# Kernel optimization log

Hardware: AMD Instinct MI355X
Metric: run time of the kernel (lower is better)

## Reference

```python
import jax, jax.numpy as jnp
import numpy as np

B, N = 4, 20                        # batch, qubits
L = int(np.ceil(np.log2(N)))        # 5 layers, one 4x4 generator each


def setup_inputs():
    key = jax.random.key(0)
    k1, k2, k3, k4 = jax.random.split(key, 4)
    psi_re = jax.random.normal(k1, (B, 2 ** N), dtype=jnp.float32)
    psi_im = jax.random.normal(k2, (B, 2 ** N), dtype=jnp.float32)
    nrm = jnp.sqrt(jnp.sum(psi_re ** 2 + psi_im ** 2, axis=1, keepdims=True))
    psi_re, psi_im = psi_re / nrm, psi_im / nrm   # normalized quantum state
    H_re = jax.random.normal(k3, (L, 4, 4), dtype=jnp.float32)
    H_im = jax.random.normal(k4, (L, 4, 4), dtype=jnp.float32)
    return {"psi_re": psi_re, "psi_im": psi_im, "H_re": H_re, "H_im": H_im}


def _make_unitary(A):
    # torch.matrix_exp(A - A^H): expm of an anti-Hermitian generator via eigh
    G = A - A.conj().T
    w, V = jnp.linalg.eigh(-1j * G)            # G = i * Hermitian
    return (V * jnp.exp(1j * w)) @ V.conj().T  # expm(G), unitary


def _apply_gate(T, U4, axes):
    # contract 4x4 gate (reshaped [2,2,2,2]) onto two qubit axes of tensor T
    T = jnp.tensordot(U4, T, axes=((2, 3), axes))
    return jnp.moveaxis(T, (0, 1), axes)


def _gate_pairs(nq):
    pairs = [(2 * i, 2 * i + 1) for i in range(nq // 2)]
    if nq > 2:
        pairs += [(2 * i + 1, (2 * i + 2) % nq) for i in range(nq // 2)]
    return pairs


def _forward(psi_re, psi_im, H_re, H_im):
    psi = (psi_re + 1j * psi_im).astype(jnp.complex64).reshape((B,) + (2,) * N)
    H = (H_re + 1j * H_im).astype(jnp.complex64)
    state, is_dm, nq = psi, False, N
    for layer in range(L):
        U = _make_unitary(H[layer]).reshape(2, 2, 2, 2)
        Uc = U.conj()
        # _2local_conv: brick pattern of the same 2-qubit gate
        for (a, b) in _gate_pairs(nq):
            state = _apply_gate(state, U, (1 + a, 1 + b))
            if is_dm:  # density matrix: also apply U* on bra axes
                state = _apply_gate(state, Uc, (1 + nq + a, 1 + nq + b))
        # _2local_pool: measuring qubits 0..nq//2-1 with index shifting removes
        # the even-indexed qubits -> partial trace over them
        if nq >= 2:
            traced = [2 * i for i in range(nq // 2)]
            kept = [q for q in range(nq) if q not in traced]
            t, k = len(traced), len(kept)
            if is_dm:
                perm = (0,) + tuple(1 + q for q in kept) + tuple(1 + q for q in traced) \
                     + tuple(1 + nq + q for q in kept) + tuple(1 + nq + q for q in traced)
                r = jnp.transpose(state, perm).reshape(B, 2 ** k, 2 ** t, 2 ** k, 2 ** t)
                state = jnp.einsum('bitjt->bij', r).reshape((B,) + (2,) * k + (2,) * k)
            else:
                perm = (0,) + tuple(1 + q for q in traced) + tuple(1 + q for q in kept)
                p = jnp.transpose(state, perm).reshape(B, 2 ** t, 2 ** k)
                state = jnp.einsum('bti,btj->bij', p, p.conj()).reshape((B,) + (2,) * k + (2,) * k)
                is_dm = True
            nq = k
    # final state.measure(0): reduced 1-qubit density matrix, take P(outcome 0)
    r = state.reshape(B, 2, 2 ** (nq - 1), 2, 2 ** (nq - 1))
    rho0 = jnp.einsum('birjr->bij', r)
    return rho0[:, 0, 0].real


def reference(psi_re, psi_im, H_re, H_im):
    return _forward(psi_re, psi_im, H_re, H_im)
```

## Files before the change

kernel.cpp:

```cpp
#include <hip/hip_runtime.h>
#include <math.h>


__device__ __forceinline__ float2 cmul(float2 a, float2 b) {
  return make_float2(a.x * b.x - a.y * b.y, a.x * b.y + a.y * b.x);
}
__device__ __forceinline__ float2 cmadd(float2 acc, float2 a, float2 b) {
  acc.x = fmaf(a.x, b.x, fmaf(-a.y, b.y, acc.x));
  acc.y = fmaf(a.x, b.y, fmaf(a.y, b.x, acc.y));
  return acc;
}
__device__ __forceinline__ float2 cmaddc(float2 acc, float2 a, float2 b) {
  acc.x = fmaf(a.x, b.x, fmaf(a.y, b.y, acc.x));
  acc.y = fmaf(a.y, b.x, fmaf(-a.x, b.y, acc.y));
  return acc;
}
__device__ __forceinline__ int pad(int e) { return e + (e >> 4); }

__device__ __forceinline__ unsigned spread(unsigned v) {
  v = (v | (v << 8)) & 0x00FF00FFu;
  v = (v | (v << 4)) & 0x0F0F0F0Fu;
  v = (v | (v << 2)) & 0x33333333u;
  v = (v | (v << 1)) & 0x55555555u;
  return v;
}
__device__ __forceinline__ unsigned spread2(unsigned v) { return spread(spread(v)); }
__device__ __forceinline__ int ins(int x, int p) {
  return ((x >> p) << (p + 1)) | (x & ((1 << p) - 1));
}

__device__ __forceinline__ void gate4(float2& v0, float2& v1, float2& v2, float2& v3,
                                      const float2 (&U)[16]) {
  float2 n0 = cmul(U[0], v0);  n0 = cmadd(n0, U[1], v1);  n0 = cmadd(n0, U[2], v2);  n0 = cmadd(n0, U[3], v3);
  float2 n1 = cmul(U[4], v0);  n1 = cmadd(n1, U[5], v1);  n1 = cmadd(n1, U[6], v2);  n1 = cmadd(n1, U[7], v3);
  float2 n2 = cmul(U[8], v0);  n2 = cmadd(n2, U[9], v1);  n2 = cmadd(n2, U[10], v2); n2 = cmadd(n2, U[11], v3);
  float2 n3 = cmul(U[12], v0); n3 = cmadd(n3, U[13], v1); n3 = cmadd(n3, U[14], v2); n3 = cmadd(n3, U[15], v3);
  v0 = n0; v1 = n1; v2 = n2; v3 = n3;
}

template <int NG>
__device__ __forceinline__ void gate16n(float2 (&v)[16], const float2 (&U)[16]) {
#pragma unroll
  for (int g = 0; g < 4; g++)
    gate4(v[g * 4 + 0], v[g * 4 + 1], v[g * 4 + 2], v[g * 4 + 3], U);
#pragma unroll
  for (int lo = 0; lo < 4; lo++)
    gate4(v[lo], v[lo + 4], v[lo + 8], v[lo + 12], U);
  if (NG == 3) {
#pragma unroll
    for (int b3 = 0; b3 < 2; b3++)
#pragma unroll
      for (int b0 = 0; b0 < 2; b0++) {
        int j = b3 * 8 + b0;
        gate4(v[j], v[j + 2], v[j + 4], v[j + 6], U);
      }
  }
}

__device__ __forceinline__ void apply_gate_tile13(float2* t, const float2 (&U)[16],
                                                  int pa, int pb, int tid) {
  int p0 = pa < pb ? pa : pb;
  int p1 = pa < pb ? pb : pa;
  int m0 = (1 << p0) - 1, m1 = (1 << p1) - 1;
  int ia = 1 << pa, ib = 1 << pb;
#pragma unroll
  for (int g = tid; g < 2048; g += 512) {
    int idx = ((g & ~m0) << 1) | (g & m0);
    idx = ((idx & ~m1) << 1) | (idx & m1);
    int e0 = pad(idx), e1 = pad(idx | ib), e2 = pad(idx | ia), e3 = pad(idx | ia | ib);
    float2 v0 = t[e0], v1 = t[e1], v2 = t[e2], v3 = t[e3];
    gate4(v0, v1, v2, v3, U);
    t[e0] = v0; t[e1] = v1; t[e2] = v2; t[e3] = v3;
  }
}

template <int NG>
__device__ __forceinline__ void phase4_l0(float2* t, const float2 (&U)[16],
                                          int p0, int p1, int p2, int p3, int tid) {
  int o0 = 1 << p0, o1 = 1 << p1, o2 = 1 << p2, o3 = 1 << p3;
  int idx = ins(ins(ins(ins(tid, p0), p1), p2), p3);
  float2 v[16];
#pragma unroll
  for (int j = 0; j < 16; j++) {
    int off = ((j & 1) ? o0 : 0) + ((j & 2) ? o1 : 0) + ((j & 4) ? o2 : 0) + ((j & 8) ? o3 : 0);
    v[j] = t[pad(idx + off)];
  }
  gate16n<NG>(v, U);
#pragma unroll
  for (int j = 0; j < 16; j++) {
    int off = ((j & 1) ? o0 : 0) + ((j & 2) ? o1 : 0) + ((j & 4) ? o2 : 0) + ((j & 8) ? o3 : 0);
    t[pad(idx + off)] = v[j];
  }
}

template <int NG>
__device__ __forceinline__ void phase4_pool(float2* w, const float2 (&U)[16],
                                            int a_lo, int a_hi, int c_lo, int c_hi,
                                            int o0, int o1, int o2, int o3, int tid) {
  int uu = tid & 7, ss = (tid >> 3) & 7, t_lo = tid >> 6;
  int u = ins(ins(uu, a_lo), a_hi);
  int s = ins(ins(ss, c_lo), c_hi);
  int base = t_lo * 1056 + s * 33 + u;
  float2 v[16];
#pragma unroll
  for (int j = 0; j < 16; j++) {
    int off = ((j & 1) ? o0 : 0) + ((j & 2) ? o1 : 0) + ((j & 4) ? o2 : 0) + ((j & 8) ? o3 : 0);
    v[j] = w[base + off];
  }
  gate16n<NG>(v, U);
#pragma unroll
  for (int j = 0; j < 16; j++) {
    int off = ((j & 1) ? o0 : 0) + ((j & 2) ? o1 : 0) + ((j & 4) ? o2 : 0) + ((j & 8) ? o3 : 0);
    w[base + off] = v[j];
  }
}

__device__ __forceinline__ void pool_p3(float2* w, const float2 (&U)[16], int tid) {
#pragma unroll
  for (int it = 0; it < 2; it++) {
    int h = tid + it * 512;
    int uu = h & 7, ss = (h >> 3) & 15, t_lo = h >> 7;
    int base = t_lo * 1056 + (ss << 1) * 33 + (uu << 2);
    float2 v[8];
    v[0] = w[base];      v[1] = w[base + 1];
    v[4] = w[base + 2];  v[5] = w[base + 3];
    v[2] = w[base + 33]; v[3] = w[base + 34];
    v[6] = w[base + 35]; v[7] = w[base + 36];
    gate4(v[0], v[1], v[2], v[3], U);
    gate4(v[4], v[5], v[6], v[7], U);
    gate4(v[0], v[2], v[4], v[6], U);
    gate4(v[1], v[3], v[5], v[7], U);
    w[base] = v[0];      w[base + 1] = v[1];
    w[base + 2] = v[4];  w[base + 3] = v[5];
    w[base + 33] = v[2]; w[base + 34] = v[3];
    w[base + 35] = v[6]; w[base + 36] = v[7];
  }
}

__global__ __launch_bounds__(320) void expm_kernel(const float* __restrict__ Hre,
                                                   const float* __restrict__ Him,
                                                   float2* __restrict__ Uout) {
  int wave = threadIdx.x >> 6;
  int lane = threadIdx.x & 63;
  if (wave >= 5 || lane >= 16) return;
  int l = wave;
  int r = lane >> 2, c = lane & 3;
  double tr = (double)Hre[l * 16 + r * 4 + c] - (double)Hre[l * 16 + c * 4 + r];
  double ti = (double)Him[l * 16 + r * 4 + c] + (double)Him[l * 16 + c * 4 + r];
  double a = sqrt(tr * tr + ti * ti);
  a += __shfl_xor(a, 1, 64);
  a += __shfl_xor(a, 2, 64);
  double nrm = fmax(a, __shfl_xor(a, 4, 64));
  nrm = fmax(nrm, __shfl_xor(nrm, 8, 64));
  int s = 0;
  while (nrm > 0.25 && s < 60) { nrm *= 0.5; s++; }
  double sc = ldexp(1.0, -s);
  tr *= sc; ti *= sc;
  double id = (r == c) ? 1.0 : 0.0;
  double er = id, ei = 0.0, pr = id, pi = 0.0;
  for (int k = 1; k <= 16; k++) {
    double qr = 0.0, qi = 0.0;
#pragma unroll
    for (int m = 0; m < 4; m++) {
      double pmr = __shfl(pr, r * 4 + m, 64);
      double pmi = __shfl(pi, r * 4 + m, 64);
      double tmr = __shfl(tr, m * 4 + c, 64);
      double tmi = __shfl(ti, m * 4 + c, 64);
      qr = fma(pmr, tmr, fma(-pmi, tmi, qr));
      qi = fma(pmr, tmi, fma(pmi, tmr, qi));
    }
    double inv = 1.0 / (double)k;
    pr = qr * inv; pi = qi * inv;
    er += pr; ei += pi;
  }
  for (int it = 0; it < s; it++) {
    double qr = 0.0, qi = 0.0;
#pragma unroll
    for (int m = 0; m < 4; m++) {
      double amr = __shfl(er, r * 4 + m, 64);
      double ami = __shfl(ei, r * 4 + m, 64);
      double bmr = __shfl(er, m * 4 + c, 64);
      double bmi = __shfl(ei, m * 4 + c, 64);
      qr = fma(amr, bmr, fma(-ami, bmi, qr));
      qi = fma(amr, bmi, fma(ami, bmr, qi));
    }
    er = qr; ei = qi;
  }
  Uout[l * 16 + lane] = make_float2((float)er, (float)ei);
}

__global__ __launch_bounds__(512, 4) void l0_pass1(const float* __restrict__ pre,
                                                   const float* __restrict__ pim,
                                                   const float2* __restrict__ Umat,
                                                   float2* __restrict__ state) {
  extern __shared__ float2 tile[];
  int tid = threadIdx.x;
  int bid = blockIdx.x;
  int b = bid >> 7, hi = bid & 127;
  size_t base = ((size_t)b << 20) | ((size_t)hi << 13);
  float2 U[16];
#pragma unroll
  for (int k = 0; k < 16; k++) U[k] = Umat[k];
  for (int e = tid; e < 8192; e += 512)
    tile[pad(e)] = make_float2(pre[base + e], pim[base + e]);
  __syncthreads();
  phase4_l0<3>(tile, U, 0, 1, 2, 3, tid);   __syncthreads();
  phase4_l0<3>(tile, U, 4, 5, 6, 7, tid);   __syncthreads();
  phase4_l0<3>(tile, U, 8, 9, 10, 11, tid); __syncthreads();
  phase4_l0<2>(tile, U, 3, 4, 7, 8, tid);   __syncthreads();
  for (int e = tid; e < 8192; e += 512) state[base + e] = tile[pad(e)];
}

__global__ __launch_bounds__(512, 4) void l0_pass2(const float2* __restrict__ Umat,
                                                   float2* __restrict__ state) {
  extern __shared__ float2 tile[];
  int tid = threadIdx.x;
  int bid = blockIdx.x;
  int b = bid >> 7, mid = bid & 127;
  size_t base = ((size_t)b << 20) | ((size_t)mid << 4);
  float2 U[16];
#pragma unroll
  for (int k = 0; k < 16; k++) U[k] = Umat[k];
  for (int e = tid; e < 8192; e += 512) {
    size_t a = base + (((size_t)(e >> 4)) << 11) + (size_t)(e & 15);
    tile[pad(e)] = state[a];
  }
  __syncthreads();
  phase4_l0<3>(tile, U, 5, 6, 7, 8, tid);    __syncthreads();
  phase4_l0<3>(tile, U, 9, 10, 11, 12, tid); __syncthreads();
  phase4_l0<2>(tile, U, 4, 5, 8, 9, tid);    __syncthreads();
  apply_gate_tile13(tile, U, 0, 12, tid);    __syncthreads();
  for (int e = tid; e < 8192; e += 512) {
    size_t a = base + (((size_t)(e >> 4)) << 11) + (size_t)(e & 15);
    state[a] = tile[pad(e)];
  }
}

__global__ __launch_bounds__(512, 4) void pool_l1(const float2* __restrict__ Umat,
                                                  const float2* __restrict__ state,
                                                  float2* __restrict__ partial) {
  extern __shared__ float2 w[];
  int tid = threadIdx.x;
  int bid = blockIdx.x;
  int b = bid >> 7, thi = bid & 127;
  size_t bbase = (size_t)b << 20;
  float2 U[16];
#pragma unroll
  for (int k = 0; k < 16; k++) U[k] = Umat[16 + k];
  unsigned tbase = spread((unsigned)(thi << 3)) << 1;
  for (int e = tid; e < 8192; e += 512) {
    int u = e & 31, s = (e >> 5) & 31, t_lo = e >> 10;
    unsigned addr = tbase | (spread((unsigned)t_lo) << 1) | spread2((unsigned)u)
                  | (spread2((unsigned)s) << 2);
    w[t_lo * 1056 + s * 33 + u] = state[bbase + (size_t)addr];
  }
  __syncthreads();
  phase4_pool<3>(w, U, 3, 4, 3, 4, 8, 264, 16, 528, tid); __syncthreads();
  phase4_pool<3>(w, U, 1, 2, 1, 2, 2, 66, 4, 132, tid);   __syncthreads();
  pool_p3(w, U, tid);                                     __syncthreads();
  phase4_pool<2>(w, U, 0, 3, 2, 4, 132, 8, 528, 1, tid);  __syncthreads();
  int wv = tid >> 6, lane = tid & 63;
  int u0 = (lane >> 3) << 2, v0 = (lane & 7) << 2;
  float2 acc[4][4];
#pragma unroll
  for (int i = 0; i < 4; i++)
#pragma unroll
    for (int j = 0; j < 4; j++) acc[i][j] = make_float2(0.f, 0.f);
  {
    int tb = wv * 1056;
#pragma unroll 4
    for (int s = 0; s < 32; s++) {
      int row = tb + s * 33;
      float2 x[4], y[4];
#pragma unroll
      for (int i = 0; i < 4; i++) { x[i] = w[row + u0 + i]; y[i] = w[row + v0 + i]; }
#pragma unroll
      for (int i = 0; i < 4; i++)
#pragma unroll
        for (int j = 0; j < 4; j++) acc[i][j] = cmaddc(acc[i][j], x[i], y[j]);
    }
  }
  __syncthreads();
  if (wv > 0) {
#pragma unroll
    for (int i = 0; i < 4; i++)
#pragma unroll
      for (int j = 0; j < 4; j++)
        w[(wv - 1) * 1024 + (u0 + i) * 32 + (v0 + j)] = acc[i][j];
  }
  __syncthreads();
  if (wv == 0) {
    float2* outp = partial + ((size_t)bid << 10);
#pragma unroll
    for (int i = 0; i < 4; i++)
#pragma unroll
      for (int j = 0; j < 4; j++) {
        float2 a = acc[i][j];
#pragma unroll
        for (int k = 0; k < 7; k++) {
          float2 o = w[k * 1024 + (u0 + i) * 32 + (v0 + j)];
          a.x += o.x; a.y += o.y;
        }
        outp[(u0 + i) * 32 + (v0 + j)] = a;
      }
  }
}

__global__ __launch_bounds__(256) void reduce_partials(const float* __restrict__ partial,
                                                       float* __restrict__ rho32) {
  int idx = blockIdx.x * 256 + threadIdx.x;
  int b = idx >> 11, p = idx & 2047;
  float acc = 0.f;
#pragma unroll 4
  for (int h = 0; h < 128; h++) acc += partial[(((size_t)(b * 128 + h)) << 11) + (size_t)p];
  rho32[idx] = acc;
}

__global__ __launch_bounds__(256) void finish(const float2* __restrict__ Umat,
                                              const float2* __restrict__ rho32,
                                              float* __restrict__ out) {
  __shared__ float2 rho[1024];
  __shared__ float2 r3s[64];
  __shared__ float2 r4s[16];
  int tid = threadIdx.x;
  int b = blockIdx.x;
  for (int p = tid; p < 1024; p += 256) rho[p] = rho32[(b << 10) + p];
  __syncthreads();

  float2 U[16], Uc[16];
#pragma unroll
  for (int k = 0; k < 16; k++) { U[k] = Umat[32 + k]; Uc[k] = make_float2(U[k].x, -U[k].y); }
  const int gl2[4][2] = {{4,3},{2,1},{3,2},{1,0}};
#pragma unroll
  for (int gi = 0; gi < 4; gi++) {
    int pa = gl2[gi][0], pb = gl2[gi][1];
    int p0 = pa < pb ? pa : pb, p1 = pa < pb ? pb : pa;
    int m0 = (1 << p0) - 1, m1 = (1 << p1) - 1;
    int ia = 1 << pa, ib = 1 << pb;
    {
      int j = tid >> 3, g = tid & 7;
      int idx = ((g & ~m0) << 1) | (g & m0);
      idx = ((idx & ~m1) << 1) | (idx & m1);
      float2 v0 = rho[idx * 32 + j], v1 = rho[(idx | ib) * 32 + j];
      float2 v2 = rho[(idx | ia) * 32 + j], v3 = rho[(idx | ia | ib) * 32 + j];
      gate4(v0, v1, v2, v3, U);
      rho[idx * 32 + j] = v0; rho[(idx | ib) * 32 + j] = v1;
      rho[(idx | ia) * 32 + j] = v2; rho[(idx | ia | ib) * 32 + j] = v3;
    }
    __syncthreads();
    {
      int i = tid >> 3, g = tid & 7;
      int idx = ((g & ~m0) << 1) | (g & m0);
      idx = ((idx & ~m1) << 1) | (idx & m1);
      float2 v0 = rho[i * 32 + idx], v1 = rho[i * 32 + (idx | ib)];
      float2 v2 = rho[i * 32 + (idx | ia)], v3 = rho[i * 32 + (idx | ia | ib)];
      gate4(v0, v1, v2, v3, Uc);
      rho[i * 32 + idx] = v0; rho[i * 32 + (idx | ib)] = v1;
      rho[i * 32 + (idx | ia)] = v2; rho[i * 32 + (idx | ia | ib)] = v3;
    }
    __syncthreads();
  }
  if (tid < 64) {
    int u = tid >> 3, v = tid & 7;
    float2 acc = {0.f, 0.f};
#pragma unroll
    for (int s = 0; s < 4; s++) {
      int iu = ((s >> 1) << 4) | ((u >> 2) << 3) | ((s & 1) << 2) | (((u >> 1) & 1) << 1) | (u & 1);
      int iv = ((s >> 1) << 4) | ((v >> 2) << 3) | ((s & 1) << 2) | (((v >> 1) & 1) << 1) | (v & 1);
      float2 x = rho[iu * 32 + iv];
      acc.x += x.x; acc.y += x.y;
    }
    r3s[u * 8 + v] = acc;
  }
  __syncthreads();

#pragma unroll
  for (int k = 0; k < 16; k++) { U[k] = Umat[48 + k]; Uc[k] = make_float2(U[k].x, -U[k].y); }
  const int gl3[2][2] = {{2,1},{1,0}};
#pragma unroll
  for (int gi = 0; gi < 2; gi++) {
    int pa = gl3[gi][0], pb = gl3[gi][1];
    int p0 = pa < pb ? pa : pb, p1 = pa < pb ? pb : pa;
    int m0 = (1 << p0) - 1, m1 = (1 << p1) - 1;
    int ia = 1 << pa, ib = 1 << pb;
    if (tid < 16) {
      int j = tid >> 1, g = tid & 1;
      int idx = ((g & ~m0) << 1) | (g & m0);
      idx = ((idx & ~m1) << 1) | (idx & m1);
      float2 v0 = r3s[idx * 8 + j], v1 = r3s[(idx | ib) * 8 + j];
      float2 v2 = r3s[(idx | ia) * 8 + j], v3 = r3s[(idx | ia | ib) * 8 + j];
      gate4(v0, v1, v2, v3, U);
      r3s[idx * 8 + j] = v0; r3s[(idx | ib) * 8 + j] = v1;
      r3s[(idx | ia) * 8 + j] = v2; r3s[(idx | ia | ib) * 8 + j] = v3;
    }
    __syncthreads();
    if (tid < 16) {
      int i = tid >> 1, g = tid & 1;
      int idx = ((g & ~m0) << 1) | (g & m0);
      idx = ((idx & ~m1) << 1) | (idx & m1);
      float2 v0 = r3s[i * 8 + idx], v1 = r3s[i * 8 + (idx | ib)];
      float2 v2 = r3s[i * 8 + (idx | ia)], v3 = r3s[i * 8 + (idx | ia | ib)];
      gate4(v0, v1, v2, v3, Uc);
      r3s[i * 8 + idx] = v0; r3s[i * 8 + (idx | ib)] = v1;
      r3s[i * 8 + (idx | ia)] = v2; r3s[i * 8 + (idx | ia | ib)] = v3;
    }
    __syncthreads();
  }
  if (tid < 16) {
    int u = tid >> 2, v = tid & 3;
    float2 acc = {0.f, 0.f};
#pragma unroll
    for (int s = 0; s < 2; s++) {
      float2 x = r3s[((s << 2) | u) * 8 + ((s << 2) | v)];
      acc.x += x.x; acc.y += x.y;
    }
    r4s[u * 4 + v] = acc;
  }
  __syncthreads();

#pragma unroll
  for (int k = 0; k < 16; k++) { U[k] = Umat[64 + k]; Uc[k] = make_float2(U[k].x, -U[k].y); }
  if (tid < 4) {
    int j = tid;
    float2 v0 = r4s[0 * 4 + j], v1 = r4s[1 * 4 + j], v2 = r4s[2 * 4 + j], v3 = r4s[3 * 4 + j];
    gate4(v0, v1, v2, v3, U);
    r4s[0 * 4 + j] = v0; r4s[1 * 4 + j] = v1; r4s[2 * 4 + j] = v2; r4s[3 * 4 + j] = v3;
  }
  __syncthreads();
  if (tid < 4) {
    int i = tid;
    float2 v0 = r4s[i * 4 + 0], v1 = r4s[i * 4 + 1], v2 = r4s[i * 4 + 2], v3 = r4s[i * 4 + 3];
    gate4(v0, v1, v2, v3, Uc);
    r4s[i * 4 + 0] = v0; r4s[i * 4 + 1] = v1; r4s[i * 4 + 2] = v2; r4s[i * 4 + 3] = v3;
  }
  __syncthreads();
  if (tid == 0) out[b] = r4s[0].x + r4s[10].x;
}

extern "C" void kernel_launch(void* const* d_in, const int* in_sizes, int n_in,
                              void* d_out, int out_size, void* d_ws, size_t ws_size,
                              hipStream_t stream) {
  const float* psi_re = (const float*)d_in[0];
  const float* psi_im = (const float*)d_in[1];
  const float* H_re = (const float*)d_in[2];
  const float* H_im = (const float*)d_in[3];
  float* out = (float*)d_out;

  char* ws = (char*)d_ws;
  float2* Umat = (float2*)ws;
  float2* state = (float2*)(ws + 4096);
  float* partial = (float*)(ws + 4096 + ((size_t)1 << 25));
  float* rho32 = (float*)(ws + 4096 + ((size_t)1 << 25) + ((size_t)1 << 22));

  const size_t LDS_L0 = 8704 * sizeof(float2);
  const size_t LDS_POOL = 8448 * sizeof(float2);

  hipLaunchKernelGGL(expm_kernel, dim3(1), dim3(320), 0, stream, H_re, H_im, Umat);
  hipLaunchKernelGGL(l0_pass1, dim3(512), dim3(512), LDS_L0, stream,
                     psi_re, psi_im, Umat, state);
  hipLaunchKernelGGL(l0_pass2, dim3(512), dim3(512), LDS_L0, stream, Umat, state);
  hipLaunchKernelGGL(pool_l1, dim3(512), dim3(512), LDS_POOL, stream,
                     Umat, state, (float2*)partial);
  hipLaunchKernelGGL(reduce_partials, dim3(32), dim3(256), 0, stream, partial, rho32);
  hipLaunchKernelGGL(finish, dim3(4), dim3(256), 0, stream, Umat, (const float2*)rho32, out);
}
```

Baseline: 189.5 us.

## Fuse expm into first pass, vectorize global I/O, repad pool LDS tile

Removes the separate expm launch: every block of l0_pass1 computes layer-0's unitary into shared memory, and block 0 also writes all five unitaries to the workspace for later kernels. Global loads and stores in l0_pass1, l0_pass2, pool_l1 and reduce_partials switch to float4 accesses to cut memory instruction count. The pool shared tile row stride changes from 33 to 35, with all offsets updated to match. Redundant per-block double-precision expm work is added, and the new padding may change LDS bank-conflict behaviour.

New measurement: 183.9 us. -3.0%, faster.

```diff
diff --git a/kernel.cpp b/kernel.cpp
--- a/kernel.cpp
+++ b/kernel.cpp
@@ -100,7 +100,7 @@
   int uu = tid & 7, ss = (tid >> 3) & 7, t_lo = tid >> 6;
   int u = ins(ins(uu, a_lo), a_hi);
   int s = ins(ins(ss, c_lo), c_hi);
-  int base = t_lo * 1056 + s * 33 + u;
+  int base = t_lo * 1120 + s * 35 + u;
   float2 v[16];
 #pragma unroll
   for (int j = 0; j < 16; j++) {
@@ -120,38 +120,34 @@
   for (int it = 0; it < 2; it++) {
     int h = tid + it * 512;
     int uu = h & 7, ss = (h >> 3) & 15, t_lo = h >> 7;
-    int base = t_lo * 1056 + (ss << 1) * 33 + (uu << 2);
+    int base = t_lo * 1120 + (ss << 1) * 35 + (uu << 2);
     float2 v[8];
     v[0] = w[base];      v[1] = w[base + 1];
     v[4] = w[base + 2];  v[5] = w[base + 3];
-    v[2] = w[base + 33]; v[3] = w[base + 34];
-    v[6] = w[base + 35]; v[7] = w[base + 36];
+    v[2] = w[base + 35]; v[3] = w[base + 36];
+    v[6] = w[base + 37]; v[7] = w[base + 38];
     gate4(v[0], v[1], v[2], v[3], U);
     gate4(v[4], v[5], v[6], v[7], U);
     gate4(v[0], v[2], v[4], v[6], U);
     gate4(v[1], v[3], v[5], v[7], U);
     w[base] = v[0];      w[base + 1] = v[1];
     w[base + 2] = v[4];  w[base + 3] = v[5];
-    w[base + 33] = v[2]; w[base + 34] = v[3];
-    w[base + 35] = v[6]; w[base + 36] = v[7];
-  }
-}
-
-__global__ __launch_bounds__(320) void expm_kernel(const float* __restrict__ Hre,
-                                                   const float* __restrict__ Him,
-                                                   float2* __restrict__ Uout) {
-  int wave = threadIdx.x >> 6;
-  int lane = threadIdx.x & 63;
-  if (wave >= 5 || lane >= 16) return;
-  int l = wave;
-  int r = lane >> 2, c = lane & 3;
+    w[base + 35] = v[2]; w[base + 36] = v[3];
+    w[base + 37] = v[6]; w[base + 38] = v[7];
+  }
+}
+
+__device__ __forceinline__ float2 expm16(const float* __restrict__ Hre,
+                                         const float* __restrict__ Him,
+                                         int l, int l16) {
+  int r = l16 >> 2, c = l16 & 3;
   double tr = (double)Hre[l * 16 + r * 4 + c] - (double)Hre[l * 16 + c * 4 + r];
   double ti = (double)Him[l * 16 + r * 4 + c] + (double)Him[l * 16 + c * 4 + r];
   double a = sqrt(tr * tr + ti * ti);
-  a += __shfl_xor(a, 1, 64);
-  a += __shfl_xor(a, 2, 64);
-  double nrm = fmax(a, __shfl_xor(a, 4, 64));
-  nrm = fmax(nrm, __shfl_xor(nrm, 8, 64));
+  a += __shfl_xor(a, 1, 16);
+  a += __shfl_xor(a, 2, 16);
+  double nrm = fmax(a, __shfl_xor(a, 4, 16));
+  nrm = fmax(nrm, __shfl_xor(nrm, 8, 16));
   int s = 0;
   while (nrm > 0.25 && s < 60) { nrm *= 0.5; s++; }
   double sc = ldexp(1.0, -s);
@@ -162,10 +158,10 @@
     double qr = 0.0, qi = 0.0;
 #pragma unroll
     for (int m = 0; m < 4; m++) {
-      double pmr = __shfl(pr, r * 4 + m, 64);
-      double pmi = __shfl(pi, r * 4 + m, 64);
-      double tmr = __shfl(tr, m * 4 + c, 64);
-      double tmi = __shfl(ti, m * 4 + c, 64);
+      double pmr = __shfl(pr, r * 4 + m, 16);
+      double pmi = __shfl(pi, r * 4 + m, 16);
+      double tmr = __shfl(tr, m * 4 + c, 16);
+      double tmi = __shfl(ti, m * 4 + c, 16);
       qr = fma(pmr, tmr, fma(-pmi, tmi, qr));
       qi = fma(pmr, tmi, fma(pmi, tmr, qi));
     }
@@ -177,38 +173,65 @@
     double qr = 0.0, qi = 0.0;
 #pragma unroll
     for (int m = 0; m < 4; m++) {
-      double amr = __shfl(er, r * 4 + m, 64);
-      double ami = __shfl(ei, r * 4 + m, 64);
-      double bmr = __shfl(er, m * 4 + c, 64);
-      double bmi = __shfl(ei, m * 4 + c, 64);
+      double amr = __shfl(er, r * 4 + m, 16);
+      double ami = __shfl(ei, r * 4 + m, 16);
+      double bmr = __shfl(er, m * 4 + c, 16);
+      double bmi = __shfl(ei, m * 4 + c, 16);
       qr = fma(amr, bmr, fma(-ami, bmi, qr));
       qi = fma(amr, bmi, fma(ami, bmr, qi));
     }
     er = qr; ei = qi;
   }
-  Uout[l * 16 + lane] = make_float2((float)er, (float)ei);
+  return make_float2((float)er, (float)ei);
 }
 
 __global__ __launch_bounds__(512, 4) void l0_pass1(const float* __restrict__ pre,
                                                    const float* __restrict__ pim,
-                                                   const float2* __restrict__ Umat,
+                                                   const float* __restrict__ Hre,
+                                                   const float* __restrict__ Him,
+                                                   float2* __restrict__ Umat,
                                                    float2* __restrict__ state) {
   extern __shared__ float2 tile[];
+  __shared__ float2 Ush[16];
   int tid = threadIdx.x;
   int bid = blockIdx.x;
   int b = bid >> 7, hi = bid & 127;
   size_t base = ((size_t)b << 20) | ((size_t)hi << 13);
+  for (int e4 = tid; e4 < 2048; e4 += 512) {
+    int e = e4 << 2;
+    float4 re = *(const float4*)&pre[base + e];
+    float4 im = *(const float4*)&pim[base + e];
+    int d = pad(e);
+    tile[d] = make_float2(re.x, im.x);
+    tile[d + 1] = make_float2(re.y, im.y);
+    tile[d + 2] = make_float2(re.z, im.z);
+    tile[d + 3] = make_float2(re.w, im.w);
+  }
+  {
+    int wv = tid >> 6, g16 = (tid & 63) >> 4, l16 = tid & 15;
+    int layer = (wv == 0) ? g16 : ((wv == 1 && g16 == 0) ? 4 : -1);
+    if (layer == 0 || (bid == 0 && layer > 0)) {
+      float2 ue = expm16(Hre, Him, layer, l16);
+      if (layer == 0) Ush[l16] = ue;
+      if (bid == 0) Umat[layer * 16 + l16] = ue;
+    }
+  }
+  __syncthreads();
   float2 U[16];
 #pragma unroll
-  for (int k = 0; k < 16; k++) U[k] = Umat[k];
-  for (int e = tid; e < 8192; e += 512)
-    tile[pad(e)] = make_float2(pre[base + e], pim[base + e]);
-  __syncthreads();
+  for (int k = 0; k < 16; k++) U[k] = Ush[k];
   phase4_l0<3>(tile, U, 0, 1, 2, 3, tid);   __syncthreads();
   phase4_l0<3>(tile, U, 4, 5, 6, 7, tid);   __syncthreads();
   phase4_l0<3>(tile, U, 8, 9, 10, 11, tid); __syncthreads();
   phase4_l0<2>(tile, U, 3, 4, 7, 8, tid);   __syncthreads();
-  for (int e = tid; e < 8192; e += 512) state[base + e] = tile[pad(e)];
+  for (int e4 = tid; e4 < 2048; e4 += 512) {
+    int e = e4 << 2;
+    int d = pad(e);
+    float2 a = tile[d], b2 = tile[d + 1], c = tile[d + 2], d2 = tile[d + 3];
+    float4* dst = (float4*)&state[base + e];
+    dst[0] = make_float4(a.x, a.y, b2.x, b2.y);
+    dst[1] = make_float4(c.x, c.y, d2.x, d2.y);
+  }
 }
 
 __global__ __launch_bounds__(512, 4) void l0_pass2(const float2* __restrict__ Umat,
@@ -221,18 +244,30 @@
   float2 U[16];
 #pragma unroll
   for (int k = 0; k < 16; k++) U[k] = Umat[k];
-  for (int e = tid; e < 8192; e += 512) {
-    size_t a = base + (((size_t)(e >> 4)) << 11) + (size_t)(e & 15);
-    tile[pad(e)] = state[a];
+  for (int f = tid; f < 2048; f += 512) {
+    int chunk = f >> 2, q = (f & 3) << 2;
+    size_t a = base + ((size_t)chunk << 11) + q;
+    const float4* src = (const float4*)&state[a];
+    float4 v0 = src[0], v1 = src[1];
+    int d = pad(chunk * 16 + q);
+    tile[d] = make_float2(v0.x, v0.y);
+    tile[d + 1] = make_float2(v0.z, v0.w);
+    tile[d + 2] = make_float2(v1.x, v1.y);
+    tile[d + 3] = make_float2(v1.z, v1.w);
   }
   __syncthreads();
   phase4_l0<3>(tile, U, 5, 6, 7, 8, tid);    __syncthreads();
   phase4_l0<3>(tile, U, 9, 10, 11, 12, tid); __syncthreads();
   phase4_l0<2>(tile, U, 4, 5, 8, 9, tid);    __syncthreads();
   apply_gate_tile13(tile, U, 0, 12, tid);    __syncthreads();
-  for (int e = tid; e < 8192; e += 512) {
-    size_t a = base + (((size_t)(e >> 4)) << 11) + (size_t)(e & 15);
-    state[a] = tile[pad(e)];
+  for (int f = tid; f < 2048; f += 512) {
+    int chunk = f >> 2, q = (f & 3) << 2;
+    size_t a = base + ((size_t)chunk << 11) + q;
+    int d = pad(chunk * 16 + q);
+    float2 x0 = tile[d], x1 = tile[d + 1], x2 = tile[d + 2], x3 = tile[d + 3];
+    float4* dst = (float4*)&state[a];
+    dst[0] = make_float4(x0.x, x0.y, x1.x, x1.y);
+    dst[1] = make_float4(x2.x, x2.y, x3.x, x3.y);
   }
 }
 
@@ -248,17 +283,20 @@
 #pragma unroll
   for (int k = 0; k < 16; k++) U[k] = Umat[16 + k];
   unsigned tbase = spread((unsigned)(thi << 3)) << 1;
-  for (int e = tid; e < 8192; e += 512) {
-    int u = e & 31, s = (e >> 5) & 31, t_lo = e >> 10;
-    unsigned addr = tbase | (spread((unsigned)t_lo) << 1) | spread2((unsigned)u)
+  for (int f = tid; f < 4096; f += 512) {
+    int up = f & 15, s = (f >> 4) & 31, t_lo = f >> 9;
+    unsigned addr = tbase | (spread((unsigned)t_lo) << 1) | (spread2((unsigned)up) << 4)
                   | (spread2((unsigned)s) << 2);
-    w[t_lo * 1056 + s * 33 + u] = state[bbase + (size_t)addr];
-  }
-  __syncthreads();
-  phase4_pool<3>(w, U, 3, 4, 3, 4, 8, 264, 16, 528, tid); __syncthreads();
-  phase4_pool<3>(w, U, 1, 2, 1, 2, 2, 66, 4, 132, tid);   __syncthreads();
+    float4 v = *(const float4*)&state[bbase + (size_t)addr];
+    int c = t_lo * 1120 + s * 35 + (up << 1);
+    w[c] = make_float2(v.x, v.y);
+    w[c + 1] = make_float2(v.z, v.w);
+  }
+  __syncthreads();
+  phase4_pool<3>(w, U, 3, 4, 3, 4, 8, 280, 16, 560, tid); __syncthreads();
+  phase4_pool<3>(w, U, 1, 2, 1, 2, 2, 70, 4, 140, tid);   __syncthreads();
   pool_p3(w, U, tid);                                     __syncthreads();
-  phase4_pool<2>(w, U, 0, 3, 2, 4, 132, 8, 528, 1, tid);  __syncthreads();
+  phase4_pool<2>(w, U, 0, 3, 2, 4, 140, 8, 560, 1, tid);  __syncthreads();
   int wv = tid >> 6, lane = tid & 63;
   int u0 = (lane >> 3) << 2, v0 = (lane & 7) << 2;
   float2 acc[4][4];
@@ -267,10 +305,10 @@
 #pragma unroll
     for (int j = 0; j < 4; j++) acc[i][j] = make_float2(0.f, 0.f);
   {
-    int tb = wv * 1056;
+    int tb = wv * 1120;
 #pragma unroll 4
     for (int s = 0; s < 32; s++) {
-      int row = tb + s * 33;
+      int row = tb + s * 35;
       float2 x[4], y[4];
 #pragma unroll
       for (int i = 0; i < 4; i++) { x[i] = w[row + u0 + i]; y[i] = w[row + v0 + i]; }
@@ -306,14 +344,17 @@
   }
 }
 
-__global__ __launch_bounds__(256) void reduce_partials(const float* __restrict__ partial,
-                                                       float* __restrict__ rho32) {
-  int idx = blockIdx.x * 256 + threadIdx.x;
-  int b = idx >> 11, p = idx & 2047;
-  float acc = 0.f;
+__global__ __launch_bounds__(256) void reduce_partials(const float4* __restrict__ partial,
+                                                       float4* __restrict__ rho32) {
+  int gid = blockIdx.x * 256 + threadIdx.x;
+  int b = gid >> 9, p = gid & 511;
+  float4 acc = make_float4(0.f, 0.f, 0.f, 0.f);
 #pragma unroll 4
-  for (int h = 0; h < 128; h++) acc += partial[(((size_t)(b * 128 + h)) << 11) + (size_t)p];
-  rho32[idx] = acc;
+  for (int h = 0; h < 128; h++) {
+    float4 v = partial[(((b << 7) + h) << 9) + p];
+    acc.x += v.x; acc.y += v.y; acc.z += v.z; acc.w += v.w;
+  }
+  rho32[gid] = acc;
 }
 
 __global__ __launch_bounds__(256) void finish(const float2* __restrict__ Umat,
@@ -453,14 +494,16 @@
   float* rho32 = (float*)(ws + 4096 + ((size_t)1 << 25) + ((size_t)1 << 22));
 
   const size_t LDS_L0 = 8704 * sizeof(float2);
-  const size_t LDS_POOL = 8448 * sizeof(float2);
-
-  hipLaunchKernelGGL(expm_kernel, dim3(1), dim3(320), 0, stream, H_re, H_im, Umat);
+  const size_t LDS_POOL = 8960 * sizeof(float2);
+
   hipLaunchKernelGGL(l0_pass1, dim3(512), dim3(512), LDS_L0, stream,
-                     psi_re, psi_im, Umat, state);
-  hipLaunchKernelGGL(l0_pass2, dim3(512), dim3(512), LDS_L0, stream, Umat, state);
+                     psi_re, psi_im, H_re, H_im, Umat, state);
+  hipLaunchKernelGGL(l0_pass2, dim3(512), dim3(512), LDS_L0, stream,
+                     (const float2*)Umat, state);
   hipLaunchKernelGGL(pool_l1, dim3(512), dim3(512), LDS_POOL, stream,
-                     Umat, state, (float2*)partial);
-  hipLaunchKernelGGL(reduce_partials, dim3(32), dim3(256), 0, stream, partial, rho32);
-  hipLaunchKernelGGL(finish, dim3(4), dim3(256), 0, stream, Umat, (const float2*)rho32, out);
-}
+                     (const float2*)Umat, (const float2*)state, (float2*)partial);
+  hipLaunchKernelGGL(reduce_partials, dim3(8), dim3(256), 0, stream,
+                     (const float4*)partial, (float4*)rho32);
+  hipLaunchKernelGGL(finish, dim3(4), dim3(256), 0, stream,
+                     (const float2*)Umat, (const float2*)rho32, out);
+}
```
